# Kernel optimization log

Hardware: AMD Instinct MI355X
Metric: run time of the kernel (lower is better)

## Reference

```python
import jax, jax.numpy as jnp
import numpy as np

EMB_SIZE = 256  # VQ embedding_size
BETA = 0.25     # commitment cost


def _mlp(x, W1, b1, W2, b2, W3, b3):
    h = jax.nn.relu(x @ W1 + b1)
    h = jax.nn.relu(h @ W2 + b2)
    return h @ W3 + b3


def setup_inputs() -> dict:
    key = jax.random.key(0)
    ks = jax.random.split(key, 5)
    B, D = 1024, 1024
    s = 1.0 / np.sqrt(D)
    return {
        "observation": jax.random.normal(ks[0], (B, D), jnp.float32),
        "W1": jax.random.normal(ks[1], (D, D), jnp.float32) * s,
        "b1": jnp.zeros((D,), jnp.float32),
        "W2": jax.random.normal(ks[2], (D, D), jnp.float32) * s,
        "b2": jnp.zeros((D,), jnp.float32),
        "W3": jax.random.normal(ks[3], (D, D), jnp.float32) * s,
        "b3": jnp.zeros((D,), jnp.float32),
        "codebook": jax.random.normal(ks[4], (512, EMB_SIZE), jnp.float32),
    }


def reference(observation, W1, b1, W2, b2, W3, b3, codebook):
    # Dense encoder
    features = _mlp(observation, W1, b1, W2, b2, W3, b3)  # [B, 1024]
    # Flatten features into embedding_size-dim tokens: [B*4, 256]
    z = features.reshape(-1, EMB_SIZE)
    # Squared euclidean distances to codebook: [N, K]
    d = (jnp.sum(z * z, axis=1, keepdims=True)
         - 2.0 * (z @ codebook.T)
         + jnp.sum(codebook * codebook, axis=1)[None, :])
    idx = jnp.argmin(d, axis=1)                   # [N] nearest code indices
    quantized = codebook[idx]                     # [N, 256] gather
    # VQ losses
    commitment_loss = jnp.mean((jax.lax.stop_gradient(quantized) - z) ** 2)
    codebook_loss = jnp.mean((quantized - jax.lax.stop_gradient(z)) ** 2)
    loss = codebook_loss + BETA * commitment_loss
    # Straight-through estimator
    quantized_st = z + jax.lax.stop_gradient(quantized - z)
    out = quantized_st.reshape(features.shape)    # [B, 1024]
    return out, loss, idx
```

## Files before the change

### kernel.cpp

```cpp
#include <hip/hip_runtime.h>


typedef _Float16 half8 __attribute__((ext_vector_type(8)));
typedef _Float16 half4 __attribute__((ext_vector_type(4)));
typedef float floatx4 __attribute__((ext_vector_type(4)));

#define LO_SCALE 2048.0f
#define INV_LO_SCALE (1.0f / 2048.0f)

__device__ __forceinline__ void gl_lds16(const _Float16* g, _Float16* l)
{
    __builtin_amdgcn_global_load_lds(
        (const __attribute__((address_space(1))) void*)g,
        (__attribute__((address_space(3))) void*)l, 16, 0, 0);
}

__device__ __forceinline__ half8 rfrag(const _Float16* m, int row, int ks, int fg)
{
    const int sw = row & 7;
    const int c1 = ((ks << 2) + (fg >> 1)) ^ sw;
    const int c2 = ((ks << 2) + (fg >> 1) + 2) ^ sw;
    const int hs = (fg & 1) << 2;
    const int rb = row << 6;
    half4 x = *reinterpret_cast<const half4*>(&m[rb + (c1 << 3) + hs]);
    half4 y = *reinterpret_cast<const half4*>(&m[rb + (c2 << 3) + hs]);
    half8 r;
    r[0] = x[0]; r[1] = x[1]; r[2] = x[2]; r[3] = x[3];
    r[4] = y[0]; r[5] = y[1]; r[6] = y[2]; r[7] = y[3];
    return r;
}

template <bool RELU, bool WF32, bool WSPLIT>
__global__ __launch_bounds__(512) void gemm_k(
    const _Float16* __restrict__ Ah, const _Float16* __restrict__ Al,
    const _Float16* __restrict__ Bh, const _Float16* __restrict__ Bl,
    const float* __restrict__ bias,
    float* __restrict__ Cf, _Float16* __restrict__ Ch, _Float16* __restrict__ Cl,
    int N, int K)
{
    __shared__ __align__(16) _Float16 sm[2][4][64 * 64];

    const int tid = threadIdx.x;
    const int m0 = blockIdx.y * 64, n0 = blockIdx.x * 64;
    const int w = tid >> 6, lane = tid & 63;

    const int mat = w >> 1;
    const int half32 = (w & 1) * 32;
    const _Float16* gsrc = (mat == 0) ? Ah : (mat == 1) ? Al : (mat == 2) ? Bh : Bl;
    const int rb0 = (mat < 2) ? m0 : n0;
    const int srow_lo = lane >> 3;
    const int sc = lane & 7;

    const int ks = w >> 2, q = w & 3;
    const int wm = (q >> 1) * 32, wn = (q & 1) * 32;
    const int fr = lane & 15, fg = lane >> 4;

    floatx4 hh[2][2] = {};
    floatx4 mx[2][2] = {};

    const int NT = K >> 6;

    auto STAGE = [&](int buf, int t) {
        const int kb = t << 6;
        #pragma unroll
        for (int j = 0; j < 4; ++j) {
            const int row = half32 + (j << 3) + srow_lo;
            const _Float16* g = gsrc + (size_t)(rb0 + row) * K + kb
                              + ((sc ^ (row & 7)) << 3);
            gl_lds16(g, &sm[buf][mat][(half32 + (j << 3)) << 6]);
        }
    };

    STAGE(0, 0);
    __syncthreads();

    for (int t = 0; t < NT; ++t) {
        const int cur = t & 1;
        if (t + 1 < NT) STAGE(cur ^ 1, t + 1);

        half8 a_h[2], a_l[2], b_h[2], b_l[2];
        #pragma unroll
        for (int i = 0; i < 2; ++i) {
            a_h[i] = rfrag(sm[cur][0], wm + (i << 4) + fr, ks, fg);
            a_l[i] = rfrag(sm[cur][1], wm + (i << 4) + fr, ks, fg);
            b_h[i] = rfrag(sm[cur][2], wn + (i << 4) + fr, ks, fg);
            b_l[i] = rfrag(sm[cur][3], wn + (i << 4) + fr, ks, fg);
        }
        #pragma unroll
        for (int i = 0; i < 2; ++i)
            #pragma unroll
            for (int j = 0; j < 2; ++j) {
                hh[i][j] = __builtin_amdgcn_mfma_f32_16x16x32_f16(a_h[i], b_h[j], hh[i][j], 0, 0, 0);
                mx[i][j] = __builtin_amdgcn_mfma_f32_16x16x32_f16(a_h[i], b_l[j], mx[i][j], 0, 0, 0);
                mx[i][j] = __builtin_amdgcn_mfma_f32_16x16x32_f16(a_l[i], b_h[j], mx[i][j], 0, 0, 0);
            }
        __syncthreads();
    }

    float* red = (float*)&sm[0][0][0];
    if (w >= 4) {
        #pragma unroll
        for (int i = 0; i < 2; ++i)
            #pragma unroll
            for (int j = 0; j < 2; ++j)
                #pragma unroll
                for (int r = 0; r < 4; ++r)
                    red[q * 1024 + ((i << 4) + (fg << 2) + r) * 32 + (j << 4) + fr]
                        = hh[i][j][r] + mx[i][j][r] * INV_LO_SCALE;
    }
    __syncthreads();
    if (w < 4) {
        #pragma unroll
        for (int j = 0; j < 2; ++j) {
            const int col = n0 + wn + (j << 4) + fr;
            const float bv = bias ? bias[col] : 0.0f;
            #pragma unroll
            for (int i = 0; i < 2; ++i)
                #pragma unroll
                for (int r = 0; r < 4; ++r) {
                    const int rl = (i << 4) + (fg << 2) + r;
                    float v = hh[i][j][r] + mx[i][j][r] * INV_LO_SCALE
                            + red[q * 1024 + rl * 32 + (j << 4) + fr] + bv;
                    if (RELU) v = fmaxf(v, 0.0f);
                    const size_t o = (size_t)(m0 + wm + rl) * N + col;
                    if (WF32) Cf[o] = v;
                    if (WSPLIT) {
                        const _Float16 hi = (_Float16)v;
                        Ch[o] = hi;
                        Cl[o] = (_Float16)((v - (float)hi) * LO_SCALE);
                    }
                }
        }
    }
}

__global__ __launch_bounds__(256) void split_kernel(
    const float* __restrict__ X, _Float16* __restrict__ H, _Float16* __restrict__ L)
{
    const int i = (blockIdx.x * 256 + threadIdx.x) * 8;
    float4 a = *reinterpret_cast<const float4*>(&X[i]);
    float4 b = *reinterpret_cast<const float4*>(&X[i + 4]);
    float xs[8] = {a.x, a.y, a.z, a.w, b.x, b.y, b.z, b.w};
    half8 h, lo;
    #pragma unroll
    for (int j = 0; j < 8; ++j) {
        const _Float16 hi = (_Float16)xs[j];
        h[j] = hi;
        lo[j] = (_Float16)((xs[j] - (float)hi) * LO_SCALE);
    }
    *reinterpret_cast<half8*>(&H[i]) = h;
    *reinterpret_cast<half8*>(&L[i]) = lo;
}

__global__ __launch_bounds__(256) void splitT3_kernel(
    const float* __restrict__ W1, const float* __restrict__ W2, const float* __restrict__ W3,
    _Float16* __restrict__ T1h, _Float16* __restrict__ T1l,
    _Float16* __restrict__ T2h, _Float16* __restrict__ T2l,
    _Float16* __restrict__ T3h, _Float16* __restrict__ T3l)
{
    const int z = blockIdx.z;
    const float* Wm = (z == 0) ? W1 : (z == 1) ? W2 : W3;
    _Float16* Th = (z == 0) ? T1h : (z == 1) ? T2h : T3h;
    _Float16* Tl = (z == 0) ? T1l : (z == 1) ? T2l : T3l;

    __shared__ float tile[64][65];
    const int tid = threadIdx.x;
    const int kb = blockIdx.y * 64, nb = blockIdx.x * 64;
    {
        const int kr = tid >> 2, c0 = (tid & 3) * 16;
        #pragma unroll
        for (int c = 0; c < 16; c += 4) {
            float4 v = *reinterpret_cast<const float4*>(
                &Wm[(size_t)(kb + kr) * 1024 + nb + c0 + c]);
            tile[kr][c0 + c] = v.x; tile[kr][c0 + c + 1] = v.y;
            tile[kr][c0 + c + 2] = v.z; tile[kr][c0 + c + 3] = v.w;
        }
    }
    __syncthreads();
    {
        const int nr = tid >> 2, k0 = (tid & 3) * 16;
        half8 h[2], lo[2];
        #pragma unroll
        for (int c = 0; c < 16; ++c) {
            const float x = tile[k0 + c][nr];
            const _Float16 hi = (_Float16)x;
            h[c >> 3][c & 7] = hi;
            lo[c >> 3][c & 7] = (_Float16)((x - (float)hi) * LO_SCALE);
        }
        const size_t o = (size_t)(nb + nr) * 1024 + kb + k0;
        *reinterpret_cast<half8*>(&Th[o]) = h[0];
        *reinterpret_cast<half8*>(&Th[o + 8]) = h[1];
        *reinterpret_cast<half8*>(&Tl[o]) = lo[0];
        *reinterpret_cast<half8*>(&Tl[o + 8]) = lo[1];
    }
}

__global__ void cb_split_kernel(const float* __restrict__ CB,
                                _Float16* __restrict__ CBh, _Float16* __restrict__ CBl,
                                float* __restrict__ cnorm)
{
    const int k = blockIdx.x, lane = threadIdx.x;
    const int i = k * 256 + lane * 4;
    float4 c = *reinterpret_cast<const float4*>(&CB[i]);
    float xs[4] = {c.x, c.y, c.z, c.w};
    half4 h, lo;
    float s = 0.f;
    #pragma unroll
    for (int j = 0; j < 4; ++j) {
        const _Float16 hi = (_Float16)xs[j];
        h[j] = hi;
        lo[j] = (_Float16)((xs[j] - (float)hi) * LO_SCALE);
        s += xs[j] * xs[j];
    }
    *reinterpret_cast<half4*>(&CBh[i]) = h;
    *reinterpret_cast<half4*>(&CBl[i]) = lo;
    #pragma unroll
    for (int off = 32; off; off >>= 1) s += __shfl_down(s, off);
    if (lane == 0) cnorm[k] = s;
}

__global__ __launch_bounds__(512) void vq_kernel(
    const _Float16* __restrict__ Fh, const _Float16* __restrict__ Fl,
    const float* __restrict__ S, const float* __restrict__ CB,
    const float* __restrict__ cnorm,
    float* __restrict__ out, float* __restrict__ pl, float* __restrict__ idx_out)
{
    const int wid = threadIdx.x >> 6, lane = threadIdx.x & 63;
    const int n = blockIdx.x * 8 + wid;

    float best = 3.4e38f;
    int bidx = 0x7fffffff;
    #pragma unroll
    for (int j = 0; j < 8; ++j) {
        const int k = j * 64 + lane;
        const float v = fmaf(-2.0f, S[(size_t)n * 512 + k], cnorm[k]);
        if (v < best) { best = v; bidx = k; }
    }
    #pragma unroll
    for (int off = 32; off; off >>= 1) {
        const float ov = __shfl_down(best, off);
        const int oi = __shfl_down(bidx, off);
        if (ov < best || (ov == best && oi < bidx)) { best = ov; bidx = oi; }
    }
    bidx = __shfl(bidx, 0);
    best = __shfl(best, 0);

    const int base = n * 256 + lane * 4;
    half4 h4 = *reinterpret_cast<const half4*>(&Fh[base]);
    half4 l4 = *reinterpret_cast<const half4*>(&Fl[base]);
    float zn = 0.f;
    #pragma unroll
    for (int j = 0; j < 4; ++j) {
        const float z = (float)h4[j] + (float)l4[j] * INV_LO_SCALE;
        zn = fmaf(z, z, zn);
    }
    #pragma unroll
    for (int off = 32; off; off >>= 1) zn += __shfl_down(zn, off);

    float4 q4 = *reinterpret_cast<const float4*>(&CB[(size_t)bidx * 256 + lane * 4]);
    *reinterpret_cast<float4*>(&out[(size_t)n * 256 + lane * 4]) = q4;

    __shared__ float part[8];
    if (lane == 0) {
        part[wid] = zn + best;
        idx_out[n] = (float)bidx;
    }
    __syncthreads();
    if (threadIdx.x == 0) {
        float s = 0.f;
        #pragma unroll
        for (int i = 0; i < 8; ++i) s += part[i];
        pl[blockIdx.x] = s;
    }
}

__global__ __launch_bounds__(512) void finalize_kernel(
    const float* __restrict__ pl, float* __restrict__ loss_out)
{
    float s = pl[threadIdx.x];
    #pragma unroll
    for (int off = 32; off; off >>= 1) s += __shfl_down(s, off);
    __shared__ float p[8];
    if ((threadIdx.x & 63) == 0) p[threadIdx.x >> 6] = s;
    __syncthreads();
    if (threadIdx.x == 0) {
        float t = 0.f;
        #pragma unroll
        for (int i = 0; i < 8; ++i) t += p[i];
        loss_out[0] = 1.25f * t / 1048576.0f;
    }
}

extern "C" void kernel_launch(void* const* d_in, const int* in_sizes, int n_in,
                              void* d_out, int out_size, void* d_ws, size_t ws_size,
                              hipStream_t stream)
{
    const float* obs = (const float*)d_in[0];
    const float* W1  = (const float*)d_in[1];
    const float* b1  = (const float*)d_in[2];
    const float* W2  = (const float*)d_in[3];
    const float* b2  = (const float*)d_in[4];
    const float* W3  = (const float*)d_in[5];
    const float* b3  = (const float*)d_in[6];
    const float* CB  = (const float*)d_in[7];

    float* out = (float*)d_out;
    float* loss_out = out + 1048576;
    float* idx_out  = out + 1048577;

    char* Wp = (char*)d_ws;
    _Float16* Oh    = (_Float16*)(Wp + (0u  << 20));
    _Float16* Ol    = (_Float16*)(Wp + (2u  << 20));
    _Float16* W1t_h = (_Float16*)(Wp + (4u  << 20));
    _Float16* W1t_l = (_Float16*)(Wp + (6u  << 20));
    _Float16* W2t_h = (_Float16*)(Wp + (8u  << 20));
    _Float16* W2t_l = (_Float16*)(Wp + (10u << 20));
    _Float16* W3t_h = (_Float16*)(Wp + (12u << 20));
    _Float16* W3t_l = (_Float16*)(Wp + (14u << 20));
    _Float16* H1_h  = (_Float16*)(Wp + (16u << 20));
    _Float16* H1_l  = (_Float16*)(Wp + (18u << 20));
    _Float16* H2_h  = (_Float16*)(Wp + (20u << 20));
    _Float16* H2_l  = (_Float16*)(Wp + (22u << 20));
    _Float16* F_h   = (_Float16*)(Wp + (24u << 20));
    _Float16* F_l   = (_Float16*)(Wp + (26u << 20));
    float*    S     = (float*)(Wp + (28u << 20));
    _Float16* CB_h  = (_Float16*)(Wp + (36u << 20));
    _Float16* CB_l  = (_Float16*)(Wp + (36u << 20) + 512 * 256 * 2);
    float*    cn    = (float*)(Wp + (36u << 20) + 2 * 512 * 256 * 2);
    float*    pl    = cn + 512;

    split_kernel<<<512, 256, 0, stream>>>(obs, Oh, Ol);
    splitT3_kernel<<<dim3(16, 16, 3), 256, 0, stream>>>(
        W1, W2, W3, W1t_h, W1t_l, W2t_h, W2t_l, W3t_h, W3t_l);
    cb_split_kernel<<<512, 64, 0, stream>>>(CB, CB_h, CB_l, cn);

    gemm_k<true, false, true><<<dim3(16, 16), 512, 0, stream>>>(
        Oh, Ol, W1t_h, W1t_l, b1, nullptr, H1_h, H1_l, 1024, 1024);
    gemm_k<true, false, true><<<dim3(16, 16), 512, 0, stream>>>(
        H1_h, H1_l, W2t_h, W2t_l, b2, nullptr, H2_h, H2_l, 1024, 1024);
    gemm_k<false, false, true><<<dim3(16, 16), 512, 0, stream>>>(
        H2_h, H2_l, W3t_h, W3t_l, b3, nullptr, F_h, F_l, 1024, 1024);
    gemm_k<false, true, false><<<dim3(8, 64), 512, 0, stream>>>(
        F_h, F_l, CB_h, CB_l, nullptr, S, nullptr, nullptr, 512, 256);

    vq_kernel<<<512, 512, 0, stream>>>(F_h, F_l, S, CB, cn, out, pl, idx_out);
    finalize_kernel<<<1, 512, 0, stream>>>(pl, loss_out);
}
```

Before: 147.6 us.

## Retile GEMMs to 32x64 blocks, permute K layout, and fuse prep kernels

The GEMM tile shrinks to 32x64 with 256 threads and no intra-block split-K. That removes the LDS reduction epilogue and doubles the block count across the CUs. Operands are written in a permuted K order, so each MFMA fragment is read as one 16-byte LDS load instead of two 8-byte loads. The three fp32-to-fp16 hi/lo split kernels are merged into one launch. The risk is that a smaller tile means less data reuse per block, and the consumers of F must stay consistent with its permuted column layout.

Result: faster. 140.3 us (-4.9%).

```diff
diff --git a/kernel.cpp b/kernel.cpp
--- a/kernel.cpp
+++ b/kernel.cpp
@@ -8,6 +8,15 @@
 #define LO_SCALE 2048.0f
 #define INV_LO_SCALE (1.0f / 2048.0f)
 
+__device__ __forceinline__ int remap4(int k0)
+{
+    return (k0 & 32) | ((k0 & 12) << 1) | ((k0 & 16) >> 2);
+}
+__device__ __forceinline__ int remap1(int k)
+{
+    return (k & ~63) | (k & 32) | ((k & 12) << 1) | ((k & 16) >> 2) | (k & 3);
+}
+
 __device__ __forceinline__ void gl_lds16(const _Float16* g, _Float16* l)
 {
     __builtin_amdgcn_global_load_lds(
@@ -17,57 +26,47 @@
 
 __device__ __forceinline__ half8 rfrag(const _Float16* m, int row, int ks, int fg)
 {
-    const int sw = row & 7;
-    const int c1 = ((ks << 2) + (fg >> 1)) ^ sw;
-    const int c2 = ((ks << 2) + (fg >> 1) + 2) ^ sw;
-    const int hs = (fg & 1) << 2;
-    const int rb = row << 6;
-    half4 x = *reinterpret_cast<const half4*>(&m[rb + (c1 << 3) + hs]);
-    half4 y = *reinterpret_cast<const half4*>(&m[rb + (c2 << 3) + hs]);
-    half8 r;
-    r[0] = x[0]; r[1] = x[1]; r[2] = x[2]; r[3] = x[3];
-    r[4] = y[0]; r[5] = y[1]; r[6] = y[2]; r[7] = y[3];
-    return r;
+    const int ch = ((ks << 2) + fg) ^ (row & 7);
+    return *reinterpret_cast<const half8*>(&m[(row << 6) + (ch << 3)]);
 }
 
 template <bool RELU, bool WF32, bool WSPLIT>
-__global__ __launch_bounds__(512) void gemm_k(
+__global__ __launch_bounds__(256) void gemm_k(
     const _Float16* __restrict__ Ah, const _Float16* __restrict__ Al,
     const _Float16* __restrict__ Bh, const _Float16* __restrict__ Bl,
     const float* __restrict__ bias,
     float* __restrict__ Cf, _Float16* __restrict__ Ch, _Float16* __restrict__ Cl,
     int N, int K)
 {
-    __shared__ __align__(16) _Float16 sm[2][4][64 * 64];
+    __shared__ __align__(16) _Float16 sm[2][192 * 64];
 
     const int tid = threadIdx.x;
-    const int m0 = blockIdx.y * 64, n0 = blockIdx.x * 64;
+    const int m0 = blockIdx.y * 32, n0 = blockIdx.x * 64;
     const int w = tid >> 6, lane = tid & 63;
-
-    const int mat = w >> 1;
-    const int half32 = (w & 1) * 32;
-    const _Float16* gsrc = (mat == 0) ? Ah : (mat == 1) ? Al : (mat == 2) ? Bh : Bl;
-    const int rb0 = (mat < 2) ? m0 : n0;
-    const int srow_lo = lane >> 3;
-    const int sc = lane & 7;
-
-    const int ks = w >> 2, q = w & 3;
-    const int wm = (q >> 1) * 32, wn = (q & 1) * 32;
+    const int srow = lane >> 3, sc = lane & 7;
+
+    const int wm = (w & 1) * 16, wn = (w >> 1) * 32;
     const int fr = lane & 15, fg = lane >> 4;
 
-    floatx4 hh[2][2] = {};
-    floatx4 mx[2][2] = {};
+    floatx4 hh[2] = {};
+    floatx4 m1[2] = {};
+    floatx4 m2[2] = {};
 
     const int NT = K >> 6;
 
     auto STAGE = [&](int buf, int t) {
         const int kb = t << 6;
         #pragma unroll
-        for (int j = 0; j < 4; ++j) {
-            const int row = half32 + (j << 3) + srow_lo;
-            const _Float16* g = gsrc + (size_t)(rb0 + row) * K + kb
-                              + ((sc ^ (row & 7)) << 3);
-            gl_lds16(g, &sm[buf][mat][(half32 + (j << 3)) << 6]);
+        for (int s = 0; s < 6; ++s) {
+            const int task = w * 6 + s;
+            const _Float16* gb;
+            int grow, lrow;
+            if (task < 4)       { gb = Ah; grow = m0 + task * 8;        lrow = task * 8; }
+            else if (task < 8)  { gb = Al; grow = m0 + (task - 4) * 8;  lrow = 32 + (task - 4) * 8; }
+            else if (task < 16) { gb = Bh; grow = n0 + (task - 8) * 8;  lrow = 64 + (task - 8) * 8; }
+            else                { gb = Bl; grow = n0 + (task - 16) * 8; lrow = 128 + (task - 16) * 8; }
+            const _Float16* g = gb + (size_t)(grow + srow) * K + kb + ((sc ^ srow) << 3);
+            gl_lds16(g, &sm[buf][lrow << 6]);
         }
     };
 
@@ -77,146 +76,139 @@
     for (int t = 0; t < NT; ++t) {
         const int cur = t & 1;
         if (t + 1 < NT) STAGE(cur ^ 1, t + 1);
-
-        half8 a_h[2], a_l[2], b_h[2], b_l[2];
-        #pragma unroll
-        for (int i = 0; i < 2; ++i) {
-            a_h[i] = rfrag(sm[cur][0], wm + (i << 4) + fr, ks, fg);
-            a_l[i] = rfrag(sm[cur][1], wm + (i << 4) + fr, ks, fg);
-            b_h[i] = rfrag(sm[cur][2], wn + (i << 4) + fr, ks, fg);
-            b_l[i] = rfrag(sm[cur][3], wn + (i << 4) + fr, ks, fg);
-        }
-        #pragma unroll
-        for (int i = 0; i < 2; ++i)
-            #pragma unroll
-            for (int j = 0; j < 2; ++j) {
-                hh[i][j] = __builtin_amdgcn_mfma_f32_16x16x32_f16(a_h[i], b_h[j], hh[i][j], 0, 0, 0);
-                mx[i][j] = __builtin_amdgcn_mfma_f32_16x16x32_f16(a_h[i], b_l[j], mx[i][j], 0, 0, 0);
-                mx[i][j] = __builtin_amdgcn_mfma_f32_16x16x32_f16(a_l[i], b_h[j], mx[i][j], 0, 0, 0);
+        const _Float16* S0 = sm[cur];
+        #pragma unroll
+        for (int ks = 0; ks < 2; ++ks) {
+            const half8 a_h  = rfrag(S0, wm + fr, ks, fg);
+            const half8 a_l  = rfrag(S0, 32 + wm + fr, ks, fg);
+            const half8 b_h0 = rfrag(S0, 64 + wn + fr, ks, fg);
+            const half8 b_h1 = rfrag(S0, 64 + wn + 16 + fr, ks, fg);
+            const half8 b_l0 = rfrag(S0, 128 + wn + fr, ks, fg);
+            const half8 b_l1 = rfrag(S0, 128 + wn + 16 + fr, ks, fg);
+            hh[0] = __builtin_amdgcn_mfma_f32_16x16x32_f16(a_h, b_h0, hh[0], 0, 0, 0);
+            hh[1] = __builtin_amdgcn_mfma_f32_16x16x32_f16(a_h, b_h1, hh[1], 0, 0, 0);
+            m1[0] = __builtin_amdgcn_mfma_f32_16x16x32_f16(a_h, b_l0, m1[0], 0, 0, 0);
+            m1[1] = __builtin_amdgcn_mfma_f32_16x16x32_f16(a_h, b_l1, m1[1], 0, 0, 0);
+            m2[0] = __builtin_amdgcn_mfma_f32_16x16x32_f16(a_l, b_h0, m2[0], 0, 0, 0);
+            m2[1] = __builtin_amdgcn_mfma_f32_16x16x32_f16(a_l, b_h1, m2[1], 0, 0, 0);
+        }
+        __syncthreads();
+    }
+
+    #pragma unroll
+    for (int j = 0; j < 2; ++j) {
+        const int col = n0 + wn + j * 16 + fr;
+        const float bv = bias ? bias[col] : 0.0f;
+        const int colr = remap1(col);
+        #pragma unroll
+        for (int r = 0; r < 4; ++r) {
+            const int row = m0 + wm + fg * 4 + r;
+            float v = hh[j][r] + (m1[j][r] + m2[j][r]) * INV_LO_SCALE + bv;
+            if (RELU) v = fmaxf(v, 0.0f);
+            if (WF32) Cf[(size_t)row * N + col] = v;
+            if (WSPLIT) {
+                const size_t o = (size_t)row * N + colr;
+                const _Float16 hi = (_Float16)v;
+                Ch[o] = hi;
+                Cl[o] = (_Float16)((v - (float)hi) * LO_SCALE);
             }
-        __syncthreads();
-    }
-
-    float* red = (float*)&sm[0][0][0];
-    if (w >= 4) {
-        #pragma unroll
-        for (int i = 0; i < 2; ++i)
-            #pragma unroll
-            for (int j = 0; j < 2; ++j)
-                #pragma unroll
-                for (int r = 0; r < 4; ++r)
-                    red[q * 1024 + ((i << 4) + (fg << 2) + r) * 32 + (j << 4) + fr]
-                        = hh[i][j][r] + mx[i][j][r] * INV_LO_SCALE;
-    }
-    __syncthreads();
-    if (w < 4) {
-        #pragma unroll
-        for (int j = 0; j < 2; ++j) {
-            const int col = n0 + wn + (j << 4) + fr;
-            const float bv = bias ? bias[col] : 0.0f;
-            #pragma unroll
-            for (int i = 0; i < 2; ++i)
-                #pragma unroll
-                for (int r = 0; r < 4; ++r) {
-                    const int rl = (i << 4) + (fg << 2) + r;
-                    float v = hh[i][j][r] + mx[i][j][r] * INV_LO_SCALE
-                            + red[q * 1024 + rl * 32 + (j << 4) + fr] + bv;
-                    if (RELU) v = fmaxf(v, 0.0f);
-                    const size_t o = (size_t)(m0 + wm + rl) * N + col;
-                    if (WF32) Cf[o] = v;
-                    if (WSPLIT) {
-                        const _Float16 hi = (_Float16)v;
-                        Ch[o] = hi;
-                        Cl[o] = (_Float16)((v - (float)hi) * LO_SCALE);
-                    }
-                }
-        }
-    }
-}
-
-__global__ __launch_bounds__(256) void split_kernel(
-    const float* __restrict__ X, _Float16* __restrict__ H, _Float16* __restrict__ L)
-{
-    const int i = (blockIdx.x * 256 + threadIdx.x) * 8;
-    float4 a = *reinterpret_cast<const float4*>(&X[i]);
-    float4 b = *reinterpret_cast<const float4*>(&X[i + 4]);
-    float xs[8] = {a.x, a.y, a.z, a.w, b.x, b.y, b.z, b.w};
-    half8 h, lo;
-    #pragma unroll
-    for (int j = 0; j < 8; ++j) {
-        const _Float16 hi = (_Float16)xs[j];
-        h[j] = hi;
-        lo[j] = (_Float16)((xs[j] - (float)hi) * LO_SCALE);
-    }
-    *reinterpret_cast<half8*>(&H[i]) = h;
-    *reinterpret_cast<half8*>(&L[i]) = lo;
-}
-
-__global__ __launch_bounds__(256) void splitT3_kernel(
-    const float* __restrict__ W1, const float* __restrict__ W2, const float* __restrict__ W3,
+        }
+    }
+}
+
+__global__ __launch_bounds__(256) void prep_kernel(
+    const float* __restrict__ W1, const float* __restrict__ W2,
+    const float* __restrict__ W3, const float* __restrict__ obs,
+    const float* __restrict__ CB,
     _Float16* __restrict__ T1h, _Float16* __restrict__ T1l,
     _Float16* __restrict__ T2h, _Float16* __restrict__ T2l,
-    _Float16* __restrict__ T3h, _Float16* __restrict__ T3l)
-{
-    const int z = blockIdx.z;
-    const float* Wm = (z == 0) ? W1 : (z == 1) ? W2 : W3;
-    _Float16* Th = (z == 0) ? T1h : (z == 1) ? T2h : T3h;
-    _Float16* Tl = (z == 0) ? T1l : (z == 1) ? T2l : T3l;
-
+    _Float16* __restrict__ T3h, _Float16* __restrict__ T3l,
+    _Float16* __restrict__ Oh, _Float16* __restrict__ Ol,
+    _Float16* __restrict__ CBh, _Float16* __restrict__ CBl,
+    float* __restrict__ cnorm)
+{
     __shared__ float tile[64][65];
-    const int tid = threadIdx.x;
-    const int kb = blockIdx.y * 64, nb = blockIdx.x * 64;
-    {
-        const int kr = tid >> 2, c0 = (tid & 3) * 16;
-        #pragma unroll
-        for (int c = 0; c < 16; c += 4) {
-            float4 v = *reinterpret_cast<const float4*>(
-                &Wm[(size_t)(kb + kr) * 1024 + nb + c0 + c]);
-            tile[kr][c0 + c] = v.x; tile[kr][c0 + c + 1] = v.y;
-            tile[kr][c0 + c + 2] = v.z; tile[kr][c0 + c + 3] = v.w;
-        }
-    }
-    __syncthreads();
-    {
-        const int nr = tid >> 2, k0 = (tid & 3) * 16;
-        half8 h[2], lo[2];
-        #pragma unroll
-        for (int c = 0; c < 16; ++c) {
-            const float x = tile[k0 + c][nr];
-            const _Float16 hi = (_Float16)x;
-            h[c >> 3][c & 7] = hi;
-            lo[c >> 3][c & 7] = (_Float16)((x - (float)hi) * LO_SCALE);
-        }
-        const size_t o = (size_t)(nb + nr) * 1024 + kb + k0;
-        *reinterpret_cast<half8*>(&Th[o]) = h[0];
-        *reinterpret_cast<half8*>(&Th[o + 8]) = h[1];
-        *reinterpret_cast<half8*>(&Tl[o]) = lo[0];
-        *reinterpret_cast<half8*>(&Tl[o + 8]) = lo[1];
-    }
-}
-
-__global__ void cb_split_kernel(const float* __restrict__ CB,
-                                _Float16* __restrict__ CBh, _Float16* __restrict__ CBl,
-                                float* __restrict__ cnorm)
-{
-    const int k = blockIdx.x, lane = threadIdx.x;
-    const int i = k * 256 + lane * 4;
-    float4 c = *reinterpret_cast<const float4*>(&CB[i]);
-    float xs[4] = {c.x, c.y, c.z, c.w};
-    half4 h, lo;
-    float s = 0.f;
-    #pragma unroll
-    for (int j = 0; j < 4; ++j) {
-        const _Float16 hi = (_Float16)xs[j];
-        h[j] = hi;
-        lo[j] = (_Float16)((xs[j] - (float)hi) * LO_SCALE);
-        s += xs[j] * xs[j];
-    }
-    *reinterpret_cast<half4*>(&CBh[i]) = h;
-    *reinterpret_cast<half4*>(&CBl[i]) = lo;
-    #pragma unroll
-    for (int off = 32; off; off >>= 1) s += __shfl_down(s, off);
-    if (lane == 0) cnorm[k] = s;
+    const int b = blockIdx.x, tid = threadIdx.x;
+
+    if (b < 768) {
+        const int z = b >> 8, rem = b & 255;
+        const float* Wm = (z == 0) ? W1 : (z == 1) ? W2 : W3;
+        _Float16* Th = (z == 0) ? T1h : (z == 1) ? T2h : T3h;
+        _Float16* Tl = (z == 0) ? T1l : (z == 1) ? T2l : T3l;
+        const int nb = (rem & 15) * 64, kb = (rem >> 4) * 64;
+        {
+            const int kr = tid >> 2, c0 = (tid & 3) * 16;
+            #pragma unroll
+            for (int c = 0; c < 16; c += 4) {
+                float4 v = *reinterpret_cast<const float4*>(
+                    &Wm[(size_t)(kb + kr) * 1024 + nb + c0 + c]);
+                tile[kr][c0 + c] = v.x; tile[kr][c0 + c + 1] = v.y;
+                tile[kr][c0 + c + 2] = v.z; tile[kr][c0 + c + 3] = v.w;
+            }
+        }
+        __syncthreads();
+        {
+            const int nr = tid >> 2, k0 = (tid & 3) * 16;
+            #pragma unroll
+            for (int g = 0; g < 4; ++g) {
+                const int kk = k0 + g * 4;
+                half4 h, lo;
+                #pragma unroll
+                for (int j = 0; j < 4; ++j) {
+                    const float x = tile[kk + j][nr];
+                    const _Float16 hi = (_Float16)x;
+                    h[j] = hi;
+                    lo[j] = (_Float16)((x - (float)hi) * LO_SCALE);
+                }
+                const size_t o = (size_t)(nb + nr) * 1024 + kb + remap4(kk);
+                *reinterpret_cast<half4*>(&Th[o]) = h;
+                *reinterpret_cast<half4*>(&Tl[o]) = lo;
+            }
+        }
+    } else if (b < 1280) {
+        const size_t e0 = ((size_t)(b - 768) * 256 + tid) * 8;
+        float4 a = *reinterpret_cast<const float4*>(&obs[e0]);
+        float4 c = *reinterpret_cast<const float4*>(&obs[e0 + 4]);
+        float xs[8] = {a.x, a.y, a.z, a.w, c.x, c.y, c.z, c.w};
+        half4 h[2], lo[2];
+        #pragma unroll
+        for (int q = 0; q < 2; ++q)
+            #pragma unroll
+            for (int j = 0; j < 4; ++j) {
+                const float x = xs[q * 4 + j];
+                const _Float16 hi = (_Float16)x;
+                h[q][j] = hi;
+                lo[q][j] = (_Float16)((x - (float)hi) * LO_SCALE);
+            }
+        const size_t base = e0 & ~(size_t)63;
+        const int r1 = remap4((int)(e0 & 63));
+        const int r2 = remap4((int)((e0 + 4) & 63));
+        *reinterpret_cast<half4*>(&Oh[base + r1]) = h[0];
+        *reinterpret_cast<half4*>(&Oh[base + r2]) = h[1];
+        *reinterpret_cast<half4*>(&Ol[base + r1]) = lo[0];
+        *reinterpret_cast<half4*>(&Ol[base + r2]) = lo[1];
+    } else {
+        const int wv = tid >> 6, lane = tid & 63;
+        const int code = (b - 1280) * 4 + wv;
+        const int k0 = lane * 4;
+        float4 c = *reinterpret_cast<const float4*>(&CB[(size_t)code * 256 + k0]);
+        float xs[4] = {c.x, c.y, c.z, c.w};
+        half4 h, lo;
+        float s = 0.f;
+        #pragma unroll
+        for (int j = 0; j < 4; ++j) {
+            const _Float16 hi = (_Float16)xs[j];
+            h[j] = hi;
+            lo[j] = (_Float16)((xs[j] - (float)hi) * LO_SCALE);
+            s += xs[j] * xs[j];
+        }
+        const size_t o = (size_t)code * 256 + (k0 & ~63) + remap4(k0 & 63);
+        *reinterpret_cast<half4*>(&CBh[o]) = h;
+        *reinterpret_cast<half4*>(&CBl[o]) = lo;
+        #pragma unroll
+        for (int off = 32; off; off >>= 1) s += __shfl_down(s, off);
+        if (lane == 0) cnorm[code] = s;
+    }
 }
 
 __global__ __launch_bounds__(512) void vq_kernel(
@@ -329,18 +321,18 @@
     float*    cn    = (float*)(Wp + (36u << 20) + 2 * 512 * 256 * 2);
     float*    pl    = cn + 512;
 
-    split_kernel<<<512, 256, 0, stream>>>(obs, Oh, Ol);
-    splitT3_kernel<<<dim3(16, 16, 3), 256, 0, stream>>>(
-        W1, W2, W3, W1t_h, W1t_l, W2t_h, W2t_l, W3t_h, W3t_l);
-    cb_split_kernel<<<512, 64, 0, stream>>>(CB, CB_h, CB_l, cn);
-
-    gemm_k<true, false, true><<<dim3(16, 16), 512, 0, stream>>>(
+    prep_kernel<<<1408, 256, 0, stream>>>(
+        W1, W2, W3, obs, CB,
+        W1t_h, W1t_l, W2t_h, W2t_l, W3t_h, W3t_l,
+        Oh, Ol, CB_h, CB_l, cn);
+
+    gemm_k<true, false, true><<<dim3(16, 32), 256, 0, stream>>>(
         Oh, Ol, W1t_h, W1t_l, b1, nullptr, H1_h, H1_l, 1024, 1024);
-    gemm_k<true, false, true><<<dim3(16, 16), 512, 0, stream>>>(
+    gemm_k<true, false, true><<<dim3(16, 32), 256, 0, stream>>>(
         H1_h, H1_l, W2t_h, W2t_l, b2, nullptr, H2_h, H2_l, 1024, 1024);
-    gemm_k<false, false, true><<<dim3(16, 16), 512, 0, stream>>>(
+    gemm_k<false, false, true><<<dim3(16, 32), 256, 0, stream>>>(
         H2_h, H2_l, W3t_h, W3t_l, b3, nullptr, F_h, F_l, 1024, 1024);
-    gemm_k<false, true, false><<<dim3(8, 64), 512, 0, stream>>>(
+    gemm_k<false, true, false><<<dim3(8, 128), 256, 0, stream>>>(
         F_h, F_l, CB_h, CB_l, nullptr, S, nullptr, nullptr, 512, 256);
 
     vq_kernel<<<512, 512, 0, stream>>>(F_h, F_l, S, CB, cn, out, pl, idx_out);
```
